# Optimization experiments

Hardware: AMD Instinct MI355X
Metric: run time of the kernel (lower is better)

## Reference

```python
import jax, jax.numpy as jnp
import numpy as np

WS = 8          # window_size
HEADS = 6
DH = 32         # dim_head


def _dwconv(t, w):
    # t: (B,C,H,W), w: (C,1,3,3) depthwise, stride 1, padding 1 -> SAME
    return jax.lax.conv_general_dilated(
        t, w, window_strides=(1, 1), padding='SAME',
        feature_group_count=t.shape[1],
        dimension_numbers=('NCHW', 'OIHW', 'NCHW'))


def _l2norm(t, eps=1e-12):
    # matches F.normalize: x / max(||x||, eps)
    n = jnp.sqrt(jnp.sum(t * t, axis=-1, keepdims=True))
    return t / jnp.maximum(n, eps)


def setup_inputs() -> dict:
    key = jax.random.key(0)
    ks = jax.random.split(key, 10)
    B, H, W, C = 2, 256, 256, 192
    s = 0.05
    return {
        'x': jax.random.normal(ks[0], (B, H, W, C), jnp.float32),
        'illu_fea_trans': jax.random.normal(ks[1], (B, H, W, C), jnp.float32),
        'gt_w': jax.random.normal(ks[2], (C, C), jnp.float32) * s,
        'gt_b': jax.random.normal(ks[3], (C,), jnp.float32) * s,
        'qkv_w': jax.random.normal(ks[4], (C, 3 * C), jnp.float32) * s,
        'qkv_b': jax.random.normal(ks[5], (3 * C,), jnp.float32) * s,
        'proj_w': jax.random.normal(ks[6], (C, C), jnp.float32) * s,
        'proj_b': jax.random.normal(ks[7], (C,), jnp.float32) * s,
        'conv1_w': jax.random.normal(ks[8], (C, 1, 3, 3), jnp.float32) * s,
        'conv2_w': jax.random.normal(ks[9], (C, 1, 3, 3), jnp.float32) * s,
    }


def reference(x, illu_fea_trans, gt_w, gt_b, qkv_w, qkv_b, proj_w, proj_b,
              conv1_w, conv2_w):
    B, H, W, C = x.shape
    Ws, heads, d = WS, HEADS, DH
    scale = d ** (-0.5)
    pad_h = (Ws - H % Ws) % Ws
    pad_w = (Ws - W % Ws) % Ws
    xp = jnp.pad(x, ((0, 0), (0, pad_h), (0, pad_w), (0, 0)), mode='reflect')
    ip = jnp.pad(illu_fea_trans, ((0, 0), (0, pad_h), (0, pad_w), (0, 0)), mode='reflect')
    Hp, Wp = xp.shape[1], xp.shape[2]
    nW = (Hp // Ws) * (Wp // Ws)
    T = Ws * Ws

    def to_windows(t):
        t = t.reshape(B, Hp // Ws, Ws, Wp // Ws, Ws, C)
        return t.transpose(0, 1, 3, 2, 4, 5).reshape(B * nW, T, C)

    xw = to_windows(xp)                                  # (B*nW, T, C)
    qkv = (xw @ qkv_w + qkv_b).reshape(B * nW, T, 3, heads, d)
    qkv = qkv.transpose(2, 0, 3, 1, 4)                   # (3, Bn, h, T, d)
    q, k, v = qkv[0], qkv[1], qkv[2]
    q = _l2norm(q)
    k = _l2norm(k)

    illu = to_windows(ip).reshape(B * nW, T, heads, d).transpose(0, 2, 1, 3)
    v = v * (1.0 + jax.nn.sigmoid(illu))

    # global token: avg-pool over padded spatial dims, then linear
    gt = jnp.mean(xp, axis=(1, 2)) @ gt_w + gt_b          # (B, C)
    gt = gt.reshape(B, heads, 1, d)
    # faithful to torch expand(dim=2 -> nW).reshape(B*nW, heads, 1, d)
    gk = jnp.broadcast_to(gt, (B, heads, nW, d)).reshape(B * nW, heads, 1, d)
    k = jnp.concatenate([k, gk], axis=2)                  # (Bn, h, T+1, d)
    v = jnp.concatenate([v, gk], axis=2)

    # chunked softmax over keys == full softmax over key axis (chunks on q only)
    attn = jax.nn.softmax(jnp.einsum('bhqd,bhkd->bhqk', q, k) * scale, axis=-1)
    out = jnp.einsum('bhqk,bhkd->bhqd', attn, v)          # (Bn, h, T, d)
    out = out.transpose(0, 2, 1, 3).reshape(B * nW, T, C)
    out = out @ proj_w + proj_b

    out = out.reshape(B, Hp // Ws, Wp // Ws, Ws, Ws, C)
    out = out.transpose(0, 1, 3, 2, 4, 5).reshape(B, Hp, Wp, C)[:, :H, :W, :]

    # depthwise-conv positional branch on padded x (exact gelu like torch)
    t = xp.transpose(0, 3, 1, 2)                          # (B,C,Hp,Wp)
    t = _dwconv(t, conv1_w)
    t = jax.nn.gelu(t, approximate=False)
    t = _dwconv(t, conv2_w)
    pos = t.transpose(0, 2, 3, 1)[:, :H, :W, :]
    return out + pos
```

## Files before the change

### kernel.cpp

```cpp
#include <hip/hip_runtime.h>
#include <hip/hip_bf16.h>

#define BB   2
#define HH   256
#define WWD  256
#define CC   192
#define WSZ  8
#define TT   64
#define NHD  6
#define DHD  32
#define N3   576

typedef __attribute__((ext_vector_type(8))) short short8;
typedef __attribute__((ext_vector_type(4))) float f32x4;

__device__ inline short bf16_bits(float f) {
  __hip_bfloat16 h = __float2bfloat16(f);
  return __builtin_bit_cast(short, h);
}

__global__ __launch_bounds__(256) void lcam_wshuf(const float* __restrict__ src,
                                                  short* __restrict__ dst,
                                                  int ncols, int nfrag) {
  int gid = blockIdx.x * 256 + threadIdx.x;
  if (gid >= nfrag) return;
  int lane = gid & 63;
  int s = (gid >> 6) % 6;
  int ct = gid / 384;
  int col = ct * 16 + (lane & 15);
  int k0 = s * 32 + (lane >> 4) * 8;
  short8 v;
#pragma unroll
  for (int j = 0; j < 8; ++j)
    v[j] = bf16_bits(src[(size_t)(k0 + j) * ncols + col]);
  *(short8*)(dst + (size_t)gid * 8) = v;
}

__global__ __launch_bounds__(256) void lcam_sum_x(const float* __restrict__ x,
                                                  float* __restrict__ sums) {
  int blk = blockIdx.x;
  int b = blk >> 9;
  int chunk = blk & 511;
  const float* xp = x + ((size_t)b * 65536 + (size_t)chunk * 128) * CC;
  int t = threadIdx.x;
  if (t < CC) {
    float acc = 0.f;
    for (int p = 0; p < 128; ++p) acc += xp[(size_t)p * CC + t];
    atomicAdd(&sums[b * CC + t], acc);
  }
}

__global__ void lcam_gt(const float* __restrict__ sums,
                        const float* __restrict__ gt_w,
                        const float* __restrict__ gt_b,
                        float* __restrict__ gt) {
  int b = blockIdx.x;
  int co = threadIdx.x;
  float acc = gt_b[co];
  const float inv = 1.f / 65536.f;
  for (int c = 0; c < CC; ++c)
    acc += sums[b * CC + c] * inv * gt_w[c * CC + co];
  gt[b * CC + co] = acc;
}

__global__ __launch_bounds__(256) void lcam_attn(
    const float* __restrict__ x, const float* __restrict__ illu,
    const short* __restrict__ wf, const short* __restrict__ pwf,
    const float* __restrict__ qkv_b, const float* __restrict__ proj_b,
    const float* __restrict__ gt, float* __restrict__ out) {
  __shared__ __align__(16) short qs[64 * 40];
  __shared__ __align__(16) short ks[80 * 40];
  __shared__ __align__(16) short vt[32 * 72];
  __shared__ __align__(16) short ps[64 * 88];
  __shared__ __align__(16) short os[64 * 200];

  int w = blockIdx.x;
  int b  = w >> 10;
  int wy = (w >> 5) & 31;
  int wx = w & 31;
  int t  = threadIdx.x;
  int lane = t & 63;
  int rtile = t >> 6;
  int m = lane & 15;
  int quad = lane >> 4;
  int key0 = rtile * 16 + quad * 4;

  size_t base = ((size_t)(b * HH + wy * WSZ) * WWD + wx * WSZ) * CC;

  int apix = rtile * 16 + m;
  size_t arow = base + (size_t)((apix >> 3) * WWD + (apix & 7)) * CC + quad * 8;
  short8 afrag[6];
#pragma unroll
  for (int s = 0; s < 6; ++s) {
    const float* ap = x + arow + s * 32;
    float4 f0 = *(const float4*)(ap);
    float4 f1 = *(const float4*)(ap + 4);
    short8 v;
    v[0] = bf16_bits(f0.x); v[1] = bf16_bits(f0.y);
    v[2] = bf16_bits(f0.z); v[3] = bf16_bits(f0.w);
    v[4] = bf16_bits(f1.x); v[5] = bf16_bits(f1.y);
    v[6] = bf16_bits(f1.z); v[7] = bf16_bits(f1.w);
    afrag[s] = v;
  }
  const short8* wf8 = (const short8*)wf;
  const short8* pwf8 = (const short8*)pwf;

  for (int h = 0; h < NHD; ++h) {
    __syncthreads();
    {
      f32x4 a0 = {0.f,0.f,0.f,0.f}, a1 = {0.f,0.f,0.f,0.f};
#pragma unroll
      for (int s = 0; s < 6; ++s)
        a0 = __builtin_amdgcn_mfma_f32_16x16x32_bf16(afrag[s], wf8[(2*h)*384 + s*64 + lane], a0, 0,0,0);
#pragma unroll
      for (int s = 0; s < 6; ++s)
        a1 = __builtin_amdgcn_mfma_f32_16x16x32_bf16(afrag[s], wf8[(2*h+1)*384 + s*64 + lane], a1, 0,0,0);
      float b0 = qkv_b[h*32 + m], b1 = qkv_b[h*32 + 16 + m];
#pragma unroll
      for (int r = 0; r < 4; ++r) {
        float v0 = a0[r] + b0, v1 = a1[r] + b1;
        float ss = v0*v0 + v1*v1;
        ss += __shfl_xor(ss, 1); ss += __shfl_xor(ss, 2);
        ss += __shfl_xor(ss, 4); ss += __shfl_xor(ss, 8);
        float scl = 0.17677669529663688f / fmaxf(sqrtf(ss), 1e-12f);
        int row = key0 + r;
        qs[row*40 + m]      = bf16_bits(v0 * scl);
        qs[row*40 + 16 + m] = bf16_bits(v1 * scl);
      }
    }
    {
      f32x4 a0 = {0.f,0.f,0.f,0.f}, a1 = {0.f,0.f,0.f,0.f};
#pragma unroll
      for (int s = 0; s < 6; ++s)
        a0 = __builtin_amdgcn_mfma_f32_16x16x32_bf16(afrag[s], wf8[(12+2*h)*384 + s*64 + lane], a0, 0,0,0);
#pragma unroll
      for (int s = 0; s < 6; ++s)
        a1 = __builtin_amdgcn_mfma_f32_16x16x32_bf16(afrag[s], wf8[(13+2*h)*384 + s*64 + lane], a1, 0,0,0);
      float b0 = qkv_b[192 + h*32 + m], b1 = qkv_b[192 + h*32 + 16 + m];
#pragma unroll
      for (int r = 0; r < 4; ++r) {
        float v0 = a0[r] + b0, v1 = a1[r] + b1;
        float ss = v0*v0 + v1*v1;
        ss += __shfl_xor(ss, 1); ss += __shfl_xor(ss, 2);
        ss += __shfl_xor(ss, 4); ss += __shfl_xor(ss, 8);
        float scl = 1.f / fmaxf(sqrtf(ss), 1e-12f);
        int row = key0 + r;
        ks[row*40 + m]      = bf16_bits(v0 * scl);
        ks[row*40 + 16 + m] = bf16_bits(v1 * scl);
      }
    }
    {
      f32x4 a0 = {0.f,0.f,0.f,0.f}, a1 = {0.f,0.f,0.f,0.f};
#pragma unroll
      for (int s = 0; s < 6; ++s)
        a0 = __builtin_amdgcn_mfma_f32_16x16x32_bf16(afrag[s], wf8[(24+2*h)*384 + s*64 + lane], a0, 0,0,0);
#pragma unroll
      for (int s = 0; s < 6; ++s)
        a1 = __builtin_amdgcn_mfma_f32_16x16x32_bf16(afrag[s], wf8[(25+2*h)*384 + s*64 + lane], a1, 0,0,0);
      float b0 = qkv_b[384 + h*32 + m], b1 = qkv_b[384 + h*32 + 16 + m];
#pragma unroll
      for (int r = 0; r < 4; ++r) {
        int key = key0 + r;
        const float* ip = illu + base + (size_t)((key >> 3) * WWD + (key & 7)) * CC + h*32;
        float i0 = ip[m], i1 = ip[16 + m];
        float s0 = 1.f / (1.f + expf(-i0));
        float s1 = 1.f / (1.f + expf(-i1));
        vt[m*72 + key]        = bf16_bits((a0[r] + b0) * (1.f + s0));
        vt[(16 + m)*72 + key] = bf16_bits((a1[r] + b1) * (1.f + s1));
      }
    }
    if (t < DHD) ks[64*40 + t] = bf16_bits(gt[b*CC + h*DHD + t]);
    __syncthreads();
    short8 qa = *(const short8*)(qs + (rtile*16 + m)*40 + quad*8);
    f32x4 sc[5];
#pragma unroll
    for (int ct = 0; ct < 5; ++ct) {
      short8 kb = *(const short8*)(ks + (ct*16 + m)*40 + quad*8);
      f32x4 z = {0.f,0.f,0.f,0.f};
      sc[ct] = __builtin_amdgcn_mfma_f32_16x16x32_bf16(qa, kb, z, 0,0,0);
    }
    float p64v[4];
#pragma unroll
    for (int r = 0; r < 4; ++r) {
      float s4 = (m == 0) ? sc[4][r] : -1e30f;
      float mx = fmaxf(fmaxf(fmaxf(sc[0][r], sc[1][r]), fmaxf(sc[2][r], sc[3][r])), s4);
      mx = fmaxf(mx, __shfl_xor(mx, 1)); mx = fmaxf(mx, __shfl_xor(mx, 2));
      mx = fmaxf(mx, __shfl_xor(mx, 4)); mx = fmaxf(mx, __shfl_xor(mx, 8));
      float e0 = expf(sc[0][r] - mx), e1 = expf(sc[1][r] - mx);
      float e2 = expf(sc[2][r] - mx), e3 = expf(sc[3][r] - mx);
      float e4 = (m == 0) ? expf(s4 - mx) : 0.f;
      float sum = e0 + e1 + e2 + e3 + e4;
      sum += __shfl_xor(sum, 1); sum += __shfl_xor(sum, 2);
      sum += __shfl_xor(sum, 4); sum += __shfl_xor(sum, 8);
      float inv = 1.f / sum;
      int row = key0 + r;
      ps[row*88 + m]      = bf16_bits(e0 * inv);
      ps[row*88 + 16 + m] = bf16_bits(e1 * inv);
      ps[row*88 + 32 + m] = bf16_bits(e2 * inv);
      ps[row*88 + 48 + m] = bf16_bits(e3 * inv);
      p64v[r] = e4 * inv;
    }
    f32x4 o0 = {0.f,0.f,0.f,0.f}, o1 = {0.f,0.f,0.f,0.f};
#pragma unroll
    for (int kc = 0; kc < 2; ++kc) {
      short8 pa  = *(const short8*)(ps + (rtile*16 + m)*88 + kc*32 + quad*8);
      short8 vb0 = *(const short8*)(vt + m*72        + kc*32 + quad*8);
      short8 vb1 = *(const short8*)(vt + (16 + m)*72 + kc*32 + quad*8);
      o0 = __builtin_amdgcn_mfma_f32_16x16x32_bf16(pa, vb0, o0, 0,0,0);
      o1 = __builtin_amdgcn_mfma_f32_16x16x32_bf16(pa, vb1, o1, 0,0,0);
    }
    float gv0 = gt[b*CC + h*32 + m];
    float gv1 = gt[b*CC + h*32 + 16 + m];
#pragma unroll
    for (int r = 0; r < 4; ++r) {
      float pr = __shfl(p64v[r], lane & 48);
      int row = key0 + r;
      os[row*200 + h*32 + m]      = bf16_bits(o0[r] + pr * gv0);
      os[row*200 + h*32 + 16 + m] = bf16_bits(o1[r] + pr * gv1);
    }
  }
  __syncthreads();
  short8 af[6];
#pragma unroll
  for (int s = 0; s < 6; ++s)
    af[s] = *(const short8*)(os + (rtile*16 + m)*200 + s*32 + quad*8);
#pragma unroll
  for (int ct = 0; ct < 12; ++ct) {
    f32x4 acc = {0.f,0.f,0.f,0.f};
#pragma unroll
    for (int s = 0; s < 6; ++s)
      acc = __builtin_amdgcn_mfma_f32_16x16x32_bf16(af[s], pwf8[ct*384 + s*64 + lane], acc, 0,0,0);
    float bias = proj_b[ct*16 + m];
#pragma unroll
    for (int r = 0; r < 4; ++r) {
      int row = key0 + r;
      out[base + (size_t)((row >> 3) * WWD + (row & 7)) * CC + ct*16 + m] = acc[r] + bias;
    }
  }
}

__global__ __launch_bounds__(256) void lcam_pos(const float* __restrict__ x,
                                                const float* __restrict__ w1,
                                                const float* __restrict__ w2,
                                                float* __restrict__ out) {
  __shared__ __align__(16) float xt[20 * 20 * 16];
  __shared__ float t1[18 * 18 * 16];
  __shared__ float wl1[16 * 9], wl2[16 * 9];
  int blk = blockIdx.x;
  int cgI = blk % 12; int tmp = blk / 12;
  int tx = tmp % 16; tmp /= 16;
  int ty = tmp % 16; int b = tmp / 16;
  int c0 = cgI * 16;
  int y0 = ty * 16, x0 = tx * 16;
  int t = threadIdx.x;
  if (t < 144) { wl1[t] = w1[c0 * 9 + t]; wl2[t] = w2[c0 * 9 + t]; }
  for (int vi = t; vi < 1600; vi += 256) {
    int cc4 = vi & 3;
    int lin = vi >> 2;
    int xx = lin % 20, yy = lin / 20;
    int gy = y0 - 2 + yy, gx = x0 - 2 + xx;
    float4 v = {0.f, 0.f, 0.f, 0.f};
    if (gy >= 0 && gy < HH && gx >= 0 && gx < WWD)
      v = *(const float4*)(x + (((size_t)b * HH + gy) * WWD + gx) * CC + c0 + cc4 * 4);
    *(float4*)(xt + (yy * 20 + xx) * 16 + cc4 * 4) = v;
  }
  __syncthreads();
  for (int idx = t; idx < 5184; idx += 256) {
    int cc = idx & 15;
    int xx = (idx >> 4) % 18;
    int yy = idx / 288;
    int gy = y0 - 1 + yy, gx = x0 - 1 + xx;
    float r = 0.f;
    if (gy >= 0 && gy < HH && gx >= 0 && gx < WWD) {
#pragma unroll
      for (int ky = 0; ky < 3; ++ky)
#pragma unroll
        for (int kx = 0; kx < 3; ++kx)
          r += xt[((yy + ky) * 20 + xx + kx) * 16 + cc] * wl1[cc * 9 + ky * 3 + kx];
      r = 0.5f * r * (1.f + erff(r * 0.70710678118654752f));
    }
    t1[(yy * 18 + xx) * 16 + cc] = r;
  }
  __syncthreads();
  for (int idx = t; idx < 4096; idx += 256) {
    int cc = idx & 15;
    int xx = (idx >> 4) & 15;
    int yy = idx >> 8;
    float r = 0.f;
#pragma unroll
    for (int ky = 0; ky < 3; ++ky)
#pragma unroll
      for (int kx = 0; kx < 3; ++kx)
        r += t1[((yy + ky) * 18 + xx + kx) * 16 + cc] * wl2[cc * 9 + ky * 3 + kx];
    size_t o = (((size_t)b * HH + y0 + yy) * WWD + x0 + xx) * CC + c0 + cc;
    out[o] += r;
  }
}

extern "C" void kernel_launch(void* const* d_in, const int* in_sizes, int n_in,
                              void* d_out, int out_size, void* d_ws, size_t ws_size,
                              hipStream_t stream) {
  const float* x       = (const float*)d_in[0];
  const float* illu    = (const float*)d_in[1];
  const float* gt_w    = (const float*)d_in[2];
  const float* gt_b    = (const float*)d_in[3];
  const float* qkv_w   = (const float*)d_in[4];
  const float* qkv_b   = (const float*)d_in[5];
  const float* proj_w  = (const float*)d_in[6];
  const float* proj_b  = (const float*)d_in[7];
  const float* conv1_w = (const float*)d_in[8];
  const float* conv2_w = (const float*)d_in[9];
  float* out = (float*)d_out;

  short* wf   = (short*)d_ws;
  short* pwf  = (short*)((char*)d_ws + 221184);
  float* sums = (float*)((char*)d_ws + 221184 + 73728);
  float* gt   = sums + BB * CC;

  hipMemsetAsync(sums, 0, BB * CC * sizeof(float), stream);
  lcam_wshuf<<<54, 256, 0, stream>>>(qkv_w, wf, N3, 36 * 6 * 64);
  lcam_wshuf<<<18, 256, 0, stream>>>(proj_w, pwf, CC, 12 * 6 * 64);
  lcam_sum_x<<<1024, 256, 0, stream>>>(x, sums);
  lcam_gt<<<BB, CC, 0, stream>>>(sums, gt_w, gt_b, gt);
  lcam_attn<<<2048, 256, 0, stream>>>(x, illu, wf, pwf, qkv_b, proj_b, gt, out);
  lcam_pos<<<6144, 256, 0, stream>>>(x, conv1_w, conv2_w, out);
}
```

Baseline: 550.3 us.

## Fuse per-head output projection, double-buffer K/V, and drop softmax max pass

Accumulates the output projection per head in registers (12 accumulators), replacing the shared-memory staging of all head outputs and the final GEMM. K and V now use double buffers so one barrier per head is removed. The softmax max subtraction is dropped because q and k are L2-normalized and the logits are bounded, and normalization is deferred to the output. The illumination loads are hoisted ahead of the MFMAs, fast rsq/rcp/exp intrinsics are used, and setprio hints wrap the MFMA blocks. This raises register pressure, and the ot buffer reuse across heads relies on per-row wavefront ownership with no barrier.

```diff
diff --git a/kernel.cpp b/kernel.cpp
--- a/kernel.cpp
+++ b/kernel.cpp
@@ -69,10 +69,10 @@
     const float* __restrict__ qkv_b, const float* __restrict__ proj_b,
     const float* __restrict__ gt, float* __restrict__ out) {
   __shared__ __align__(16) short qs[64 * 40];
-  __shared__ __align__(16) short ks[80 * 40];
-  __shared__ __align__(16) short vt[32 * 72];
-  __shared__ __align__(16) short ps[64 * 88];
-  __shared__ __align__(16) short os[64 * 200];
+  __shared__ __align__(16) short ks[2][65 * 40];
+  __shared__ __align__(16) short vt[2][32 * 72];
+  __shared__ __align__(16) short ps[64 * 72];
+  __shared__ __align__(16) short ot[64 * 40];
 
   int w = blockIdx.x;
   int b  = w >> 10;
@@ -105,16 +105,36 @@
   const short8* wf8 = (const short8*)wf;
   const short8* pwf8 = (const short8*)pwf;
 
+  f32x4 pacc[12];
+#pragma unroll
+  for (int ct = 0; ct < 12; ++ct) {
+    f32x4 z = {0.f, 0.f, 0.f, 0.f};
+    pacc[ct] = z;
+  }
+
   for (int h = 0; h < NHD; ++h) {
-    __syncthreads();
+    short* ksb = ks[h & 1];
+    short* vtb = vt[h & 1];
+    float gv0 = gt[b * CC + h * 32 + m];
+    float gv1 = gt[b * CC + h * 32 + 16 + m];
+    float il0[4], il1[4];
+#pragma unroll
+    for (int r = 0; r < 4; ++r) {
+      int key = key0 + r;
+      const float* ip = illu + base + (size_t)((key >> 3) * WWD + (key & 7)) * CC + h * 32;
+      il0[r] = ip[m];
+      il1[r] = ip[16 + m];
+    }
     {
       f32x4 a0 = {0.f,0.f,0.f,0.f}, a1 = {0.f,0.f,0.f,0.f};
+      __builtin_amdgcn_s_setprio(1);
 #pragma unroll
       for (int s = 0; s < 6; ++s)
         a0 = __builtin_amdgcn_mfma_f32_16x16x32_bf16(afrag[s], wf8[(2*h)*384 + s*64 + lane], a0, 0,0,0);
 #pragma unroll
       for (int s = 0; s < 6; ++s)
         a1 = __builtin_amdgcn_mfma_f32_16x16x32_bf16(afrag[s], wf8[(2*h+1)*384 + s*64 + lane], a1, 0,0,0);
+      __builtin_amdgcn_s_setprio(0);
       float b0 = qkv_b[h*32 + m], b1 = qkv_b[h*32 + 16 + m];
 #pragma unroll
       for (int r = 0; r < 4; ++r) {
@@ -122,7 +142,7 @@
         float ss = v0*v0 + v1*v1;
         ss += __shfl_xor(ss, 1); ss += __shfl_xor(ss, 2);
         ss += __shfl_xor(ss, 4); ss += __shfl_xor(ss, 8);
-        float scl = 0.17677669529663688f / fmaxf(sqrtf(ss), 1e-12f);
+        float scl = 0.17677669529663688f * __builtin_amdgcn_rsqf(fmaxf(ss, 1e-24f));
         int row = key0 + r;
         qs[row*40 + m]      = bf16_bits(v0 * scl);
         qs[row*40 + 16 + m] = bf16_bits(v1 * scl);
@@ -130,12 +150,14 @@
     }
     {
       f32x4 a0 = {0.f,0.f,0.f,0.f}, a1 = {0.f,0.f,0.f,0.f};
+      __builtin_amdgcn_s_setprio(1);
 #pragma unroll
       for (int s = 0; s < 6; ++s)
         a0 = __builtin_amdgcn_mfma_f32_16x16x32_bf16(afrag[s], wf8[(12+2*h)*384 + s*64 + lane], a0, 0,0,0);
 #pragma unroll
       for (int s = 0; s < 6; ++s)
         a1 = __builtin_amdgcn_mfma_f32_16x16x32_bf16(afrag[s], wf8[(13+2*h)*384 + s*64 + lane], a1, 0,0,0);
+      __builtin_amdgcn_s_setprio(0);
       float b0 = qkv_b[192 + h*32 + m], b1 = qkv_b[192 + h*32 + 16 + m];
 #pragma unroll
       for (int r = 0; r < 4; ++r) {
@@ -143,98 +165,96 @@
         float ss = v0*v0 + v1*v1;
         ss += __shfl_xor(ss, 1); ss += __shfl_xor(ss, 2);
         ss += __shfl_xor(ss, 4); ss += __shfl_xor(ss, 8);
-        float scl = 1.f / fmaxf(sqrtf(ss), 1e-12f);
+        float scl = __builtin_amdgcn_rsqf(fmaxf(ss, 1e-24f));
         int row = key0 + r;
-        ks[row*40 + m]      = bf16_bits(v0 * scl);
-        ks[row*40 + 16 + m] = bf16_bits(v1 * scl);
+        ksb[row*40 + m]      = bf16_bits(v0 * scl);
+        ksb[row*40 + 16 + m] = bf16_bits(v1 * scl);
       }
     }
     {
       f32x4 a0 = {0.f,0.f,0.f,0.f}, a1 = {0.f,0.f,0.f,0.f};
+      __builtin_amdgcn_s_setprio(1);
 #pragma unroll
       for (int s = 0; s < 6; ++s)
         a0 = __builtin_amdgcn_mfma_f32_16x16x32_bf16(afrag[s], wf8[(24+2*h)*384 + s*64 + lane], a0, 0,0,0);
 #pragma unroll
       for (int s = 0; s < 6; ++s)
         a1 = __builtin_amdgcn_mfma_f32_16x16x32_bf16(afrag[s], wf8[(25+2*h)*384 + s*64 + lane], a1, 0,0,0);
+      __builtin_amdgcn_s_setprio(0);
       float b0 = qkv_b[384 + h*32 + m], b1 = qkv_b[384 + h*32 + 16 + m];
 #pragma unroll
       for (int r = 0; r < 4; ++r) {
         int key = key0 + r;
-        const float* ip = illu + base + (size_t)((key >> 3) * WWD + (key & 7)) * CC + h*32;
-        float i0 = ip[m], i1 = ip[16 + m];
-        float s0 = 1.f / (1.f + expf(-i0));
-        float s1 = 1.f / (1.f + expf(-i1));
-        vt[m*72 + key]        = bf16_bits((a0[r] + b0) * (1.f + s0));
-        vt[(16 + m)*72 + key] = bf16_bits((a1[r] + b1) * (1.f + s1));
+        float s0 = __builtin_amdgcn_rcpf(1.f + __expf(-il0[r]));
+        float s1 = __builtin_amdgcn_rcpf(1.f + __expf(-il1[r]));
+        vtb[m*72 + key]        = bf16_bits((a0[r] + b0) * (1.f + s0));
+        vtb[(16 + m)*72 + key] = bf16_bits((a1[r] + b1) * (1.f + s1));
       }
     }
-    if (t < DHD) ks[64*40 + t] = bf16_bits(gt[b*CC + h*DHD + t]);
+    if (t < DHD) ksb[64*40 + t] = bf16_bits(gt[b*CC + h*DHD + t]);
     __syncthreads();
     short8 qa = *(const short8*)(qs + (rtile*16 + m)*40 + quad*8);
     f32x4 sc[5];
 #pragma unroll
-    for (int ct = 0; ct < 5; ++ct) {
-      short8 kb = *(const short8*)(ks + (ct*16 + m)*40 + quad*8);
+    for (int ct = 0; ct < 4; ++ct) {
+      short8 kb = *(const short8*)(ksb + (ct*16 + m)*40 + quad*8);
       f32x4 z = {0.f,0.f,0.f,0.f};
       sc[ct] = __builtin_amdgcn_mfma_f32_16x16x32_bf16(qa, kb, z, 0,0,0);
     }
-    float p64v[4];
+    {
+      short8 kb = *(const short8*)(ksb + 64*40 + quad*8);
+      f32x4 z = {0.f,0.f,0.f,0.f};
+      sc[4] = __builtin_amdgcn_mfma_f32_16x16x32_bf16(qa, kb, z, 0,0,0);
+    }
+    float p64v[4], invr[4];
 #pragma unroll
     for (int r = 0; r < 4; ++r) {
-      float s4 = (m == 0) ? sc[4][r] : -1e30f;
-      float mx = fmaxf(fmaxf(fmaxf(sc[0][r], sc[1][r]), fmaxf(sc[2][r], sc[3][r])), s4);
-      mx = fmaxf(mx, __shfl_xor(mx, 1)); mx = fmaxf(mx, __shfl_xor(mx, 2));
-      mx = fmaxf(mx, __shfl_xor(mx, 4)); mx = fmaxf(mx, __shfl_xor(mx, 8));
-      float e0 = expf(sc[0][r] - mx), e1 = expf(sc[1][r] - mx);
-      float e2 = expf(sc[2][r] - mx), e3 = expf(sc[3][r] - mx);
-      float e4 = (m == 0) ? expf(s4 - mx) : 0.f;
+      float e0 = __expf(sc[0][r]), e1 = __expf(sc[1][r]);
+      float e2 = __expf(sc[2][r]), e3 = __expf(sc[3][r]);
+      float e4 = (m == 0) ? __expf(sc[4][r]) : 0.f;
+      int row = key0 + r;
+      ps[row*72 + m]      = bf16_bits(e0);
+      ps[row*72 + 16 + m] = bf16_bits(e1);
+      ps[row*72 + 32 + m] = bf16_bits(e2);
+      ps[row*72 + 48 + m] = bf16_bits(e3);
       float sum = e0 + e1 + e2 + e3 + e4;
       sum += __shfl_xor(sum, 1); sum += __shfl_xor(sum, 2);
       sum += __shfl_xor(sum, 4); sum += __shfl_xor(sum, 8);
-      float inv = 1.f / sum;
-      int row = key0 + r;
-      ps[row*88 + m]      = bf16_bits(e0 * inv);
-      ps[row*88 + 16 + m] = bf16_bits(e1 * inv);
-      ps[row*88 + 32 + m] = bf16_bits(e2 * inv);
-      ps[row*88 + 48 + m] = bf16_bits(e3 * inv);
-      p64v[r] = e4 * inv;
+      invr[r] = __builtin_amdgcn_rcpf(sum);
+      p64v[r] = e4;
     }
     f32x4 o0 = {0.f,0.f,0.f,0.f}, o1 = {0.f,0.f,0.f,0.f};
+    __builtin_amdgcn_s_setprio(1);
 #pragma unroll
     for (int kc = 0; kc < 2; ++kc) {
-      short8 pa  = *(const short8*)(ps + (rtile*16 + m)*88 + kc*32 + quad*8);
-      short8 vb0 = *(const short8*)(vt + m*72        + kc*32 + quad*8);
-      short8 vb1 = *(const short8*)(vt + (16 + m)*72 + kc*32 + quad*8);
+      short8 pa  = *(const short8*)(ps + (rtile*16 + m)*72 + kc*32 + quad*8);
+      short8 vb0 = *(const short8*)(vtb + m*72        + kc*32 + quad*8);
+      short8 vb1 = *(const short8*)(vtb + (16 + m)*72 + kc*32 + quad*8);
       o0 = __builtin_amdgcn_mfma_f32_16x16x32_bf16(pa, vb0, o0, 0,0,0);
       o1 = __builtin_amdgcn_mfma_f32_16x16x32_bf16(pa, vb1, o1, 0,0,0);
     }
-    float gv0 = gt[b*CC + h*32 + m];
-    float gv1 = gt[b*CC + h*32 + 16 + m];
+    __builtin_amdgcn_s_setprio(0);
 #pragma unroll
     for (int r = 0; r < 4; ++r) {
       float pr = __shfl(p64v[r], lane & 48);
       int row = key0 + r;
-      os[row*200 + h*32 + m]      = bf16_bits(o0[r] + pr * gv0);
-      os[row*200 + h*32 + 16 + m] = bf16_bits(o1[r] + pr * gv1);
-    }
-  }
-  __syncthreads();
-  short8 af[6];
-#pragma unroll
-  for (int s = 0; s < 6; ++s)
-    af[s] = *(const short8*)(os + (rtile*16 + m)*200 + s*32 + quad*8);
+      ot[row*40 + m]      = bf16_bits((o0[r] + pr * gv0) * invr[r]);
+      ot[row*40 + 16 + m] = bf16_bits((o1[r] + pr * gv1) * invr[r]);
+    }
+    short8 oa = *(const short8*)(ot + (rtile*16 + m)*40 + quad*8);
+    __builtin_amdgcn_s_setprio(1);
+#pragma unroll
+    for (int ct = 0; ct < 12; ++ct)
+      pacc[ct] = __builtin_amdgcn_mfma_f32_16x16x32_bf16(oa, pwf8[ct*384 + h*64 + lane], pacc[ct], 0,0,0);
+    __builtin_amdgcn_s_setprio(0);
+  }
 #pragma unroll
   for (int ct = 0; ct < 12; ++ct) {
-    f32x4 acc = {0.f,0.f,0.f,0.f};
-#pragma unroll
-    for (int s = 0; s < 6; ++s)
-      acc = __builtin_amdgcn_mfma_f32_16x16x32_bf16(af[s], pwf8[ct*384 + s*64 + lane], acc, 0,0,0);
     float bias = proj_b[ct*16 + m];
 #pragma unroll
     for (int r = 0; r < 4; ++r) {
       int row = key0 + r;
-      out[base + (size_t)((row >> 3) * WWD + (row & 7)) * CC + ct*16 + m] = acc[r] + bias;
+      out[base + (size_t)((row >> 3) * WWD + (row & 7)) * CC + ct*16 + m] = pacc[ct][r] + bias;
     }
   }
 }
```

Measured after the change: 574.7 us. 1.04x slower.
